# Optimization experiments

Hardware: AMD Instinct MI355X
Metric: run time of the kernel (lower is better)

Reference implementation:

```python
import jax, jax.numpy as jnp
import numpy as np

LAMBDA_GEO = 0.5


def setup_inputs() -> dict:
    key = jax.random.key(0)
    embeddings = jax.random.normal(key, (4, 2048, 512), dtype=jnp.float32)
    return {"embeddings": embeddings}


def _geometric_loss(embeddings):
    b, s, d = embeddings.shape
    x = embeddings.reshape(b * s, d)  # [N, d]
    sq_norm = jnp.sum(x * x, axis=-1)  # [N]
    sq = sq_norm[:, None] + sq_norm[None, :] - 2.0 * (x @ x.T)  # [N, N]
    sq = jnp.maximum(sq, 0.0)
    dist = jnp.sqrt(sq)  # torch.cdist(p=2)
    return jnp.mean(jnp.exp(-dist * 0.1)) * 0.1


def reference(embeddings):
    geometric_loss = _geometric_loss(embeddings)
    total_geometric = LAMBDA_GEO * geometric_loss
    return geometric_loss, total_geometric
```

## Files before the change

### kernel.cpp

```cpp
#include <hip/hip_runtime.h>

#define NROWS 8192
#define DIM   512
#define NT    64
#define NTRI  (NT * (NT + 1) / 2)
#define NACC  64

using f32x4 = __attribute__((ext_vector_type(4))) float;

__device__ __forceinline__ unsigned char f2e4m3(float x) {
    unsigned ux = __float_as_uint(x);
    unsigned s  = (ux >> 24) & 0x80u;
    float a = __uint_as_float(ux & 0x7FFFFFFFu);
    a = fminf(a, 448.0f);
    unsigned ua = __float_as_uint(a);
    int eb = (int)(ua >> 23);
    if (eb < 121) eb = 121;
    float step  = __uint_as_float((unsigned)(eb - 3) << 23);
    float istep = __uint_as_float((unsigned)(257 - eb) << 23);
    float q = rintf(a * istep) * step;
    q = fminf(q, 448.0f);
    if (q < 0.001953125f)
        return (unsigned char)s;
    unsigned uq = __float_as_uint(q);
    int eq = (int)(uq >> 23) - 127;
    unsigned byte;
    if (eq < -6) byte = (unsigned)(q * 512.0f);
    else         byte = (unsigned)((eq + 7) << 3) | ((uq >> 20) & 7u);
    return (unsigned char)(s | byte);
}

__global__ __launch_bounds__(256) void norm_convert_kernel(
    const float* __restrict__ X, unsigned char* __restrict__ Xq,
    float* __restrict__ norms, float* __restrict__ acc)
{
    const int tid  = threadIdx.x;
    const int lane = tid & 63;
    const int w    = tid >> 6;
    const int row  = blockIdx.x * 4 + w;

    if (blockIdx.x == 0 && tid < NACC + 1) acc[tid] = 0.0f;

    const float* xr = X + (size_t)row * DIM + lane * 8;
    float4 v0 = *(const float4*)xr;
    float4 v1 = *(const float4*)(xr + 4);

    float s = 0.0f;
    s = fmaf(v0.x, v0.x, s); s = fmaf(v0.y, v0.y, s);
    s = fmaf(v0.z, v0.z, s); s = fmaf(v0.w, v0.w, s);
    s = fmaf(v1.x, v1.x, s); s = fmaf(v1.y, v1.y, s);
    s = fmaf(v1.z, v1.z, s); s = fmaf(v1.w, v1.w, s);

    union { unsigned char b[8]; uint2 v; } pk;
    pk.b[0] = f2e4m3(v0.x); pk.b[1] = f2e4m3(v0.y);
    pk.b[2] = f2e4m3(v0.z); pk.b[3] = f2e4m3(v0.w);
    pk.b[4] = f2e4m3(v1.x); pk.b[5] = f2e4m3(v1.y);
    pk.b[6] = f2e4m3(v1.z); pk.b[7] = f2e4m3(v1.w);

    const int slab = lane >> 3;
    const int cpos = (lane & 7) ^ (row & 7);
    *(uint2*)(Xq + (size_t)row * DIM + slab * 64 + cpos * 8) = pk.v;

    #pragma unroll
    for (int off = 32; off > 0; off >>= 1) s += __shfl_down(s, off, 64);
    if (lane == 0) norms[row] = s;
}

__global__ __launch_bounds__(256, 4) void pair_loss_gemm_kernel(
    const unsigned char* __restrict__ Xq, const float* __restrict__ norms,
    float* __restrict__ acc, float* __restrict__ out)
{
    __shared__ __align__(16) char As0[8192];
    __shared__ __align__(16) char As1[8192];
    __shared__ __align__(16) char Bs0[8192];
    __shared__ __align__(16) char Bs1[8192];
    __shared__ float wsum[4];
    __shared__ int lastflag;

    int t = blockIdx.x, bi = 0;
    while (t >= (NT - bi)) { t -= (NT - bi); bi++; }
    const int bj = bi + t;

    const int tid  = threadIdx.x;
    const int lane = tid & 63;
    const int w    = tid >> 6;

    const int rowA = bi * 128;
    const int rowB = bj * 128;

    f32x4 accv[4][4];
    const f32x4 zero = {0.0f, 0.0f, 0.0f, 0.0f};
    #pragma unroll
    for (int a = 0; a < 4; a++)
        #pragma unroll
        for (int b = 0; b < 4; b++) accv[a][b] = zero;

    const int r0 = tid >> 1;
    const int h0 = tid & 1;
    const int wb = r0 * 64 + h0 * 32;
    const unsigned char* gA = Xq + (size_t)(rowA + r0) * DIM + h0 * 32;
    const unsigned char* gB = Xq + (size_t)(rowB + r0) * DIM + h0 * 32;

    const int fr  = lane & 15;
    const int q   = lane >> 4;
    const int fo0 = fr * 64 + ((q ^ (fr & 7)) * 8);
    const int wr  = (w & 1) * 64;
    const int wc  = (w >> 1) * 64;

    {
        uint4 pa0 = *(const uint4*)gA;
        uint4 pa1 = *(const uint4*)(gA + 16);
        uint4 pb0 = *(const uint4*)gB;
        uint4 pb1 = *(const uint4*)(gB + 16);
        *(uint4*)(As0 + wb)      = pa0;
        *(uint4*)(As0 + wb + 16) = pa1;
        *(uint4*)(Bs0 + wb)      = pb0;
        *(uint4*)(Bs0 + wb + 16) = pb1;
    }
    __syncthreads();

    char* curA = As0; char* nxtA = As1;
    char* curB = Bs0; char* nxtB = Bs1;

    #pragma unroll 1
    for (int k = 0; k < 8; k++) {
        uint4 pa0, pa1, pb0, pb1;
        const bool more = (k < 7);
        if (more) {
            const int k0 = (k + 1) * 64;
            pa0 = *(const uint4*)(gA + k0);
            pa1 = *(const uint4*)(gA + k0 + 16);
            pb0 = *(const uint4*)(gB + k0);
            pb1 = *(const uint4*)(gB + k0 + 16);
        }

        #pragma unroll
        for (int s = 0; s < 2; s++) {
            const int fo = fo0 ^ (s << 5);
            long af[4], bf[4];
            #pragma unroll
            for (int a = 0; a < 4; a++)
                af[a] = *(const long*)(curA + (wr + a * 16) * 64 + fo);
            #pragma unroll
            for (int b = 0; b < 4; b++)
                bf[b] = *(const long*)(curB + (wc + b * 16) * 64 + fo);
            #pragma unroll
            for (int a = 0; a < 4; a++)
                #pragma unroll
                for (int b = 0; b < 4; b++)
                    accv[a][b] = __builtin_amdgcn_mfma_f32_16x16x32_fp8_fp8(
                        af[a], bf[b], accv[a][b], 0, 0, 0);
        }

        if (more) {
            *(uint4*)(nxtA + wb)      = pa0;
            *(uint4*)(nxtA + wb + 16) = pa1;
            *(uint4*)(nxtB + wb)      = pb0;
            *(uint4*)(nxtB + wb + 16) = pb1;
            __syncthreads();
            char* tA = curA; curA = nxtA; nxtA = tA;
            char* tB = curB; curB = nxtB; nxtB = tB;
        }
    }

    const float wgt = (bi == bj) ? 1.0f : 2.0f;
    float lsum = 0.0f;
    #pragma unroll
    for (int a = 0; a < 4; a++) {
        const int gi0 = rowA + wr + a * 16 + (lane >> 4) * 4;
        #pragma unroll
        for (int b = 0; b < 4; b++) {
            const int gj = rowB + wc + b * 16 + (lane & 15);
            const float nj = norms[gj];
            #pragma unroll
            for (int r = 0; r < 4; r++) {
                const int gi = gi0 + r;
                float sq = fmaf(-2.0f, accv[a][b][r], norms[gi] + nj);
                sq = fmaxf(sq, 0.0f);
                float term = __expf(-0.1f * sqrtf(sq));
                if (gi == gj) term = 1.0f;
                lsum += term;
            }
        }
    }
    lsum *= wgt;
    #pragma unroll
    for (int off = 32; off > 0; off >>= 1) lsum += __shfl_down(lsum, off, 64);
    if (lane == 0) wsum[w] = lsum;
    __syncthreads();

    if (tid == 0) {
        float bsum = wsum[0] + wsum[1] + wsum[2] + wsum[3];
        float old = atomicAdd(&acc[blockIdx.x & (NACC - 1)], bsum);
        asm volatile("" :: "v"(old));
        unsigned prev = atomicAdd((unsigned int*)(acc + NACC), 1u);
        lastflag = (prev == NTRI - 1) ? 1 : 0;
    }
    __syncthreads();
    if (lastflag && tid < 64) {
        float v = atomicAdd(&acc[tid], 0.0f);
        #pragma unroll
        for (int off = 32; off > 0; off >>= 1) v += __shfl_down(v, off, 64);
        if (tid == 0) {
            const float inv = 1.0f / ((float)NROWS * (float)NROWS);
            float loss = v * inv * 0.1f;
            out[0] = loss;
            out[1] = 0.5f * loss;
        }
    }
}

extern "C" void kernel_launch(void* const* d_in, const int* in_sizes, int n_in,
                              void* d_out, int out_size, void* d_ws, size_t ws_size,
                              hipStream_t stream)
{
    const float* X = (const float*)d_in[0];
    float* out = (float*)d_out;

    char* ws = (char*)d_ws;
    float*         acc   = (float*)ws;
    float*         norms = (float*)(ws + 1024);
    unsigned char* Xq    = (unsigned char*)(ws + 1024 + 32768);

    norm_convert_kernel<<<NROWS / 4, 256, 0, stream>>>(X, Xq, norms, acc);
    pair_loss_gemm_kernel<<<NTRI, 256, 0, stream>>>(Xq, norms, acc, out);
}
```

Baseline: 111.2 us.

## Use persistent 256x256 tiles with ticket scheduling and direct global-to-LDS triple buffering

Replaces the one-block-per-128x128 triangle tile launch with a persistent grid of 256 blocks of 512 threads. Each block pulls 256x256 upper-triangle tiles from an atomic ticket counter. K slices are staged with global_load_lds into a triple-buffered LDS ring, with explicit waitcnt, barriers and setprio around the MFMAs, and the fp8 swizzle is changed to 16-byte granularity to match. The aim is to raise operand reuse per byte loaded, hide load latency and cut tail and launch imbalance. The cost is more barriers per step and more accumulator registers per thread, which can lower occupancy.

```diff
diff --git a/kernel.cpp b/kernel.cpp
--- a/kernel.cpp
+++ b/kernel.cpp
@@ -2,8 +2,9 @@
 
 #define NROWS 8192
 #define DIM   512
-#define NT    64
-#define NTRI  (NT * (NT + 1) / 2)
+#define NTB   32
+#define NTRI  (NTB * (NTB + 1) / 2)
+#define NGRID 256
 #define NACC  64
 
 using f32x4 = __attribute__((ext_vector_type(4))) float;
@@ -39,7 +40,7 @@
     const int w    = tid >> 6;
     const int row  = blockIdx.x * 4 + w;
 
-    if (blockIdx.x == 0 && tid < NACC + 1) acc[tid] = 0.0f;
+    if (blockIdx.x == 0 && tid < NACC + 2) acc[tid] = 0.0f;
 
     const float* xr = X + (size_t)row * DIM + lane * 8;
     float4 v0 = *(const float4*)xr;
@@ -58,143 +59,166 @@
     pk.b[6] = f2e4m3(v1.z); pk.b[7] = f2e4m3(v1.w);
 
     const int slab = lane >> 3;
-    const int cpos = (lane & 7) ^ (row & 7);
-    *(uint2*)(Xq + (size_t)row * DIM + slab * 64 + cpos * 8) = pk.v;
+    const int c16  = (lane >> 1) & 3;
+    const int cpos = c16 ^ ((row >> 1) & 3);
+    *(uint2*)(Xq + (size_t)row * DIM + slab * 64 + cpos * 16 + (lane & 1) * 8)
+        = pk.v;
 
     #pragma unroll
     for (int off = 32; off > 0; off >>= 1) s += __shfl_down(s, off, 64);
     if (lane == 0) norms[row] = s;
 }
 
-__global__ __launch_bounds__(256, 4) void pair_loss_gemm_kernel(
+__device__ __forceinline__ void gload16(const void* g, void* l) {
+    __builtin_amdgcn_global_load_lds(
+        (const __attribute__((address_space(1))) unsigned int*)g,
+        (__attribute__((address_space(3))) unsigned int*)l, 16, 0, 0);
+}
+
+__global__ __launch_bounds__(512, 2) void pair_loss_gemm_kernel(
     const unsigned char* __restrict__ Xq, const float* __restrict__ norms,
     float* __restrict__ acc, float* __restrict__ out)
 {
-    __shared__ __align__(16) char As0[8192];
-    __shared__ __align__(16) char As1[8192];
-    __shared__ __align__(16) char Bs0[8192];
-    __shared__ __align__(16) char Bs1[8192];
-    __shared__ float wsum[4];
-    __shared__ int lastflag;
-
-    int t = blockIdx.x, bi = 0;
-    while (t >= (NT - bi)) { t -= (NT - bi); bi++; }
-    const int bj = bi + t;
+    __shared__ __align__(16) char Ls[3][16384];
+    __shared__ float wsum[8];
+    __shared__ int tsh, lastflag;
 
     const int tid  = threadIdx.x;
     const int lane = tid & 63;
     const int w    = tid >> 6;
-
-    const int rowA = bi * 128;
-    const int rowB = bj * 128;
-
-    f32x4 accv[4][4];
-    const f32x4 zero = {0.0f, 0.0f, 0.0f, 0.0f};
-    #pragma unroll
-    for (int a = 0; a < 4; a++)
-        #pragma unroll
-        for (int b = 0; b < 4; b++) accv[a][b] = zero;
-
-    const int r0 = tid >> 1;
-    const int h0 = tid & 1;
-    const int wb = r0 * 64 + h0 * 32;
-    const unsigned char* gA = Xq + (size_t)(rowA + r0) * DIM + h0 * 32;
-    const unsigned char* gB = Xq + (size_t)(rowB + r0) * DIM + h0 * 32;
-
-    const int fr  = lane & 15;
-    const int q   = lane >> 4;
-    const int fo0 = fr * 64 + ((q ^ (fr & 7)) * 8);
-    const int wr  = (w & 1) * 64;
-    const int wc  = (w >> 1) * 64;
-
-    {
-        uint4 pa0 = *(const uint4*)gA;
-        uint4 pa1 = *(const uint4*)(gA + 16);
-        uint4 pb0 = *(const uint4*)gB;
-        uint4 pb1 = *(const uint4*)(gB + 16);
-        *(uint4*)(As0 + wb)      = pa0;
-        *(uint4*)(As0 + wb + 16) = pa1;
-        *(uint4*)(Bs0 + wb)      = pb0;
-        *(uint4*)(Bs0 + wb + 16) = pb1;
-    }
-    __syncthreads();
-
-    char* curA = As0; char* nxtA = As1;
-    char* curB = Bs0; char* nxtB = Bs1;
+    const int wm   = w >> 2;
+    const int wn   = w & 3;
+
+    const int fr = lane & 15;
+    const int q  = lane >> 4;
+    const int fo = fr * 32 + (((q >> 1) ^ ((fr >> 1) & 1)) * 16) + (q & 1) * 8;
+
+    const int srow = w * 32 + (lane >> 1);
+    const int w3   = (lane >> 2) & 3;
+    const int pos0 = ((lane & 1) ^ (w3 & 1)) ^ w3;
+    const int pos1 = pos0 ^ 2;
+    const int sdst = w * 1024 + lane * 16;
+
+    unsigned int* ticket = (unsigned int*)acc + NACC + 1;
+    float total = 0.0f;
 
     #pragma unroll 1
-    for (int k = 0; k < 8; k++) {
-        uint4 pa0, pa1, pb0, pb1;
-        const bool more = (k < 7);
-        if (more) {
-            const int k0 = (k + 1) * 64;
-            pa0 = *(const uint4*)(gA + k0);
-            pa1 = *(const uint4*)(gA + k0 + 16);
-            pb0 = *(const uint4*)(gB + k0);
-            pb1 = *(const uint4*)(gB + k0 + 16);
-        }
-
-        #pragma unroll
-        for (int s = 0; s < 2; s++) {
-            const int fo = fo0 ^ (s << 5);
-            long af[4], bf[4];
+    for (;;) {
+        __syncthreads();
+        if (tid == 0) tsh = (int)atomicAdd(ticket, 1u);
+        __syncthreads();
+        const int tt = tsh;
+        if (tt >= NTRI) break;
+
+        int u = tt, bi = 0;
+        while (u >= (NTB - bi)) { u -= (NTB - bi); bi++; }
+        const int bj = bi + u;
+        const int rowA = bi * 256;
+        const int rowB = bj * 256;
+
+        const unsigned char* gA = Xq + (size_t)(rowA + srow) * DIM;
+        const unsigned char* gB = Xq + (size_t)(rowB + srow) * DIM;
+
+        f32x4 accv[8][4];
+        const f32x4 zero = {0.0f, 0.0f, 0.0f, 0.0f};
+        #pragma unroll
+        for (int a = 0; a < 8; a++)
             #pragma unroll
-            for (int a = 0; a < 4; a++)
-                af[a] = *(const long*)(curA + (wr + a * 16) * 64 + fo);
+            for (int b = 0; b < 4; b++) accv[a][b] = zero;
+
+#define STG(t_, u_) do {                                                   \
+        char* d_ = Ls[(t_) % 3] + ((u_) * 8192) + sdst;                    \
+        const unsigned char* g_ = ((u_) ? gB : gA) + ((t_) >> 1) * 64      \
+                                + (((t_) & 1) ? pos1 : pos0) * 16;         \
+        gload16(g_, d_);                                                   \
+    } while (0)
+
+        STG(0, 0); STG(0, 1);
+        STG(1, 0); STG(1, 1);
+        asm volatile("s_waitcnt vmcnt(2)" ::: "memory");
+        __builtin_amdgcn_sched_barrier(0);
+        __builtin_amdgcn_s_barrier();
+        __builtin_amdgcn_sched_barrier(0);
+
+        #pragma unroll 1
+        for (int t = 0; t < 16; t++) {
+            const char* Ab = Ls[t % 3];
+            const char* Bb = Ab + 8192;
+            long bf[4];
             #pragma unroll
-            for (int b = 0; b < 4; b++)
-                bf[b] = *(const long*)(curB + (wc + b * 16) * 64 + fo);
-            #pragma unroll
-            for (int a = 0; a < 4; a++)
+            for (int p = 0; p < 2; p++) {
+                long af[4];
+                if (p == 0) {
+                    #pragma unroll
+                    for (int b = 0; b < 4; b++)
+                        bf[b] = *(const long*)(Bb + (wn * 64 + b * 16) * 32 + fo);
+                }
                 #pragma unroll
-                for (int b = 0; b < 4; b++)
-                    accv[a][b] = __builtin_amdgcn_mfma_f32_16x16x32_fp8_fp8(
-                        af[a], bf[b], accv[a][b], 0, 0, 0);
-        }
-
-        if (more) {
-            *(uint4*)(nxtA + wb)      = pa0;
-            *(uint4*)(nxtA + wb + 16) = pa1;
-            *(uint4*)(nxtB + wb)      = pb0;
-            *(uint4*)(nxtB + wb + 16) = pb1;
-            __syncthreads();
-            char* tA = curA; curA = nxtA; nxtA = tA;
-            char* tB = curB; curB = nxtB; nxtB = tB;
-        }
-    }
-
-    const float wgt = (bi == bj) ? 1.0f : 2.0f;
-    float lsum = 0.0f;
-    #pragma unroll
-    for (int a = 0; a < 4; a++) {
-        const int gi0 = rowA + wr + a * 16 + (lane >> 4) * 4;
-        #pragma unroll
-        for (int b = 0; b < 4; b++) {
-            const int gj = rowB + wc + b * 16 + (lane & 15);
-            const float nj = norms[gj];
-            #pragma unroll
-            for (int r = 0; r < 4; r++) {
-                const int gi = gi0 + r;
-                float sq = fmaf(-2.0f, accv[a][b][r], norms[gi] + nj);
-                sq = fmaxf(sq, 0.0f);
-                float term = __expf(-0.1f * sqrtf(sq));
-                if (gi == gj) term = 1.0f;
-                lsum += term;
+                for (int a = 0; a < 4; a++)
+                    af[a] = *(const long*)(Ab + (wm * 128 + p * 64 + a * 16) * 32 + fo);
+                if (t < 14) STG(t + 2, p);
+                __builtin_amdgcn_sched_barrier(0);
+                __builtin_amdgcn_s_barrier();
+                __builtin_amdgcn_sched_barrier(0);
+                __builtin_amdgcn_s_setprio(1);
+                #pragma unroll
+                for (int a = 0; a < 4; a++)
+                    #pragma unroll
+                    for (int b = 0; b < 4; b++)
+                        accv[p * 4 + a][b] =
+                            __builtin_amdgcn_mfma_f32_16x16x32_fp8_fp8(
+                                af[a], bf[b], accv[p * 4 + a][b], 0, 0, 0);
+                __builtin_amdgcn_s_setprio(0);
+                __builtin_amdgcn_sched_barrier(0);
+                if (p == 1) {
+                    if (t < 14)
+                        asm volatile("s_waitcnt vmcnt(2)" ::: "memory");
+                    else if (t == 14)
+                        asm volatile("s_waitcnt vmcnt(0)" ::: "memory");
+                }
+                __builtin_amdgcn_sched_barrier(0);
+                __builtin_amdgcn_s_barrier();
+                __builtin_amdgcn_sched_barrier(0);
             }
         }
+#undef STG
+
+        const float wgt = (bi == bj) ? 1.0f : 2.0f;
+        float lsum = 0.0f;
+        #pragma unroll
+        for (int a = 0; a < 8; a++) {
+            const int gi0 = rowA + wm * 128 + a * 16 + (lane >> 4) * 4;
+            #pragma unroll
+            for (int b = 0; b < 4; b++) {
+                const int gj = rowB + wn * 64 + b * 16 + (lane & 15);
+                const float nj = norms[gj];
+                #pragma unroll
+                for (int r = 0; r < 4; r++) {
+                    const int gi = gi0 + r;
+                    float sq = fmaf(-2.0f, accv[a][b][r], norms[gi] + nj);
+                    sq = fmaxf(sq, 0.0f);
+                    float term = __expf(-0.1f * sqrtf(sq));
+                    if (gi == gj) term = 1.0f;
+                    lsum += term;
+                }
+            }
+        }
+        total += wgt * lsum;
     }
-    lsum *= wgt;
+
     #pragma unroll
-    for (int off = 32; off > 0; off >>= 1) lsum += __shfl_down(lsum, off, 64);
-    if (lane == 0) wsum[w] = lsum;
+    for (int off = 32; off > 0; off >>= 1) total += __shfl_down(total, off, 64);
+    if (lane == 0) wsum[w] = total;
     __syncthreads();
 
     if (tid == 0) {
-        float bsum = wsum[0] + wsum[1] + wsum[2] + wsum[3];
+        float bsum = 0.0f;
+        #pragma unroll
+        for (int i = 0; i < 8; i++) bsum += wsum[i];
         float old = atomicAdd(&acc[blockIdx.x & (NACC - 1)], bsum);
         asm volatile("" :: "v"(old));
         unsigned prev = atomicAdd((unsigned int*)(acc + NACC), 1u);
-        lastflag = (prev == NTRI - 1) ? 1 : 0;
+        lastflag = (prev == NGRID - 1) ? 1 : 0;
     }
     __syncthreads();
     if (lastflag && tid < 64) {
@@ -223,5 +247,5 @@
     unsigned char* Xq    = (unsigned char*)(ws + 1024 + 32768);
 
     norm_convert_kernel<<<NROWS / 4, 256, 0, stream>>>(X, Xq, norms, acc);
-    pair_loss_gemm_kernel<<<NTRI, 256, 0, stream>>>(Xq, norms, acc, out);
-}
+    pair_loss_gemm_kernel<<<NGRID, 512, 0, stream>>>(Xq, norms, acc, out);
+}
```

Result: slower. 150.3 us (+35.2%).
